# Optimization experiments

Measured on AMD Instinct MI355X. Metric: run time of the kernel, lower is better.

## Reference

```python
import jax, jax.numpy as jnp
import numpy as np

B, K, DIM = 8, 256, 50257
KNN, N_CLASS = 8, 4
KNN_T = 0.05


def setup_inputs() -> dict:
    key = jax.random.key(0)
    k1, k2, k3 = jax.random.split(key, 3)
    # probability-like positive values so log() is finite (KL-style distance)
    logits = jax.random.uniform(k1, (B, DIM), jnp.float32, minval=1e-3, maxval=1.0)
    queue_anchor = jax.random.uniform(k2, (B, K, DIM), jnp.float32, minval=1e-3, maxval=1.0)
    queue_label = jax.random.randint(k3, (B, K), 0, N_CLASS)  # int32 labels in [0, N_CLASS)
    return {"logits": logits, "queue_anchor": queue_anchor, "queue_label": queue_label}


def reference(logits, queue_anchor, queue_label):
    # KL-style distance over the vocab dim: dists[b,k] = mean_d qa[b,k,d]*(log qa[b,k,d] - log logits[b,d])
    log_logits = jnp.log(logits)  # [B, DIM]
    dists = jnp.mean(queue_anchor * (jnp.log(queue_anchor) - log_logits[:, None, :]), axis=2)  # [B, K]
    scaled_dists = (-1.0 / KNN_T) * dists
    top_dists, top_indices = jax.lax.top_k(scaled_dists, KNN)  # [B, KNN]
    top_values = jnp.take_along_axis(queue_label, top_indices, axis=1)  # [B, KNN] class ids
    knn_weight = jax.nn.softmax(top_dists, axis=-1)  # [B, KNN]
    # scatter weight into class bins then sum over neighbors == weighted one-hot sum
    knn_prob = jnp.sum(jax.nn.one_hot(top_values, N_CLASS, dtype=knn_weight.dtype) * knn_weight[..., None], axis=1)  # [B, N_CLASS]
    return knn_prob
```

## Files before the change

### kernel.cpp

```cpp
#include <hip/hip_runtime.h>
#include <math.h>

#define BATCH 8
#define KQ 256
#define DIM 50257
#define KNN 8
#define N_CLASS 4
#define INV_T 20.0f
#define LLSTRIDE 50264

__global__ __launch_bounds__(256) void log_logits_kernel(
        const float* __restrict__ logits, float* __restrict__ ll4, int n) {
    int i = blockIdx.x * 256 + threadIdx.x;
    if (i >= n) return;
    int b = i / DIM;
    int d = i - b * DIM;
    float v = __logf(logits[i]);
    #pragma unroll
    for (int c = 0; c < 4; ++c)
        ll4[((size_t)(c * BATCH + b)) * LLSTRIDE + c + d] = v;
}

__global__ __launch_bounds__(256) void dists_kernel(
        const float* __restrict__ qa, const float* __restrict__ ll4,
        float* __restrict__ dists) {
    const int bk = blockIdx.x;
    const int b  = bk >> 8;
    const int c  = bk & 3;
    const float* __restrict__ qrow = qa  + (size_t)bk * DIM;
    const float* __restrict__ lrow = ll4 + ((size_t)(c * BATCH + b)) * LLSTRIDE + c;

    const int peel = (4 - c) & 3;
    const int nv   = (DIM - peel) >> 2;
    const int tail = peel + nv * 4;
    const int t = threadIdx.x;

    float ax = 0.f, ay = 0.f, az = 0.f, aw = 0.f;
    const float4* __restrict__ q4 = (const float4*)(qrow + peel);
    const float4* __restrict__ l4 = (const float4*)(lrow + peel);
    for (int i = t; i < nv; i += 256) {
        float4 q = q4[i];
        float4 l = l4[i];
        ax += q.x * (__logf(q.x) - l.x);
        ay += q.y * (__logf(q.y) - l.y);
        az += q.z * (__logf(q.z) - l.z);
        aw += q.w * (__logf(q.w) - l.w);
    }
    float s = (ax + ay) + (az + aw);

    if (t < peel) {
        float q = qrow[t];
        s += q * (__logf(q) - lrow[t]);
    }
    int tn = DIM - tail;
    if (t >= 4 && t < 4 + tn) {
        int d = tail + (t - 4);
        float q = qrow[d];
        s += q * (__logf(q) - lrow[d]);
    }

    for (int o = 32; o > 0; o >>= 1) s += __shfl_xor(s, o, 64);
    __shared__ float part[4];
    if ((t & 63) == 0) part[t >> 6] = s;
    __syncthreads();
    if (t == 0) {
        float tot = (part[0] + part[1]) + (part[2] + part[3]);
        dists[bk] = tot * (1.0f / (float)DIM);
    }
}

__global__ __launch_bounds__(64) void topk_kernel(
        const float* __restrict__ dists, const int* __restrict__ labels,
        float* __restrict__ out) {
    const int b = blockIdx.x;
    const int lane = threadIdx.x;
    const int base = lane * 4;
    const float* __restrict__ drow = dists + b * KQ;

    float v[4];
    #pragma unroll
    for (int j = 0; j < 4; ++j) v[j] = -INV_T * drow[base + j];

    float topv[KNN]; int topi[KNN];
    #pragma unroll
    for (int it = 0; it < KNN; ++it) {
        float lv = v[0]; int li = base;
        #pragma unroll
        for (int j = 1; j < 4; ++j)
            if (v[j] > lv || (v[j] == lv && base + j < li)) { lv = v[j]; li = base + j; }
        #pragma unroll
        for (int o = 32; o > 0; o >>= 1) {
            float ov = __shfl_xor(lv, o, 64);
            int   oi = __shfl_xor(li, o, 64);
            if (ov > lv || (ov == lv && oi < li)) { lv = ov; li = oi; }
        }
        topv[it] = lv; topi[it] = li;
        if (li >= base && li < base + 4) v[li - base] = -INFINITY;
    }

    if (lane == 0) {
        float m = topv[0];
        float w[KNN], sum = 0.f;
        #pragma unroll
        for (int i = 0; i < KNN; ++i) { w[i] = __expf(topv[i] - m); sum += w[i]; }
        float p[N_CLASS] = {0.f, 0.f, 0.f, 0.f};
        #pragma unroll
        for (int i = 0; i < KNN; ++i) p[labels[b * KQ + topi[i]]] += w[i];
        float inv = 1.0f / sum;
        #pragma unroll
        for (int c = 0; c < N_CLASS; ++c) out[b * N_CLASS + c] = p[c] * inv;
    }
}

extern "C" void kernel_launch(void* const* d_in, const int* in_sizes, int n_in,
                              void* d_out, int out_size, void* d_ws, size_t ws_size,
                              hipStream_t stream) {
    const float* logits = (const float*)d_in[0];
    const float* qa     = (const float*)d_in[1];
    const int*   labels = (const int*)d_in[2];
    float* out = (float*)d_out;

    float* ll4   = (float*)d_ws;
    float* dists = ll4 + (size_t)4 * BATCH * LLSTRIDE;

    const int n_ll = BATCH * DIM;
    log_logits_kernel<<<(n_ll + 255) / 256, 256, 0, stream>>>(logits, ll4, n_ll);
    dists_kernel<<<BATCH * KQ, 256, 0, stream>>>(qa, ll4, dists);
    topk_kernel<<<BATCH, 64, 0, stream>>>(dists, labels, out);
}
```

Measured before the change: 557.5 us.

## Halve log-logits copies, use nontemporal loads, and unroll dists loop 4x

Measured after the change: 535.7 us. 1.04x faster.

```diff
diff --git a/kernel.cpp b/kernel.cpp
--- a/kernel.cpp
+++ b/kernel.cpp
@@ -7,28 +7,35 @@
 #define KNN 8
 #define N_CLASS 4
 #define INV_T 20.0f
-#define LLSTRIDE 50264
+#define LL2STRIDE 50260
+
+typedef float vf4 __attribute__((ext_vector_type(4)));
+
+__device__ __forceinline__ vf4 nt_load4(const float* p) {
+    return __builtin_nontemporal_load((const vf4*)p);
+}
 
 __global__ __launch_bounds__(256) void log_logits_kernel(
-        const float* __restrict__ logits, float* __restrict__ ll4, int n) {
+        const float* __restrict__ logits, float* __restrict__ ll2, int n) {
     int i = blockIdx.x * 256 + threadIdx.x;
     if (i >= n) return;
     int b = i / DIM;
     int d = i - b * DIM;
     float v = __logf(logits[i]);
     #pragma unroll
-    for (int c = 0; c < 4; ++c)
-        ll4[((size_t)(c * BATCH + b)) * LLSTRIDE + c + d] = v;
+    for (int s = 0; s < 2; ++s)
+        ll2[((size_t)(s * BATCH + b)) * LL2STRIDE + s + d] = v;
 }
 
 __global__ __launch_bounds__(256) void dists_kernel(
-        const float* __restrict__ qa, const float* __restrict__ ll4,
+        const float* __restrict__ qa, const float* __restrict__ ll2,
         float* __restrict__ dists) {
     const int bk = blockIdx.x;
     const int b  = bk >> 8;
     const int c  = bk & 3;
-    const float* __restrict__ qrow = qa  + (size_t)bk * DIM;
-    const float* __restrict__ lrow = ll4 + ((size_t)(c * BATCH + b)) * LLSTRIDE + c;
+    const int s  = bk & 1;
+    const float* __restrict__ qrow  = qa  + (size_t)bk * DIM;
+    const float* __restrict__ lrow2 = ll2 + ((size_t)(s * BATCH + b)) * LL2STRIDE + s;
 
     const int peel = (4 - c) & 3;
     const int nv   = (DIM - peel) >> 2;
@@ -36,32 +43,60 @@
     const int t = threadIdx.x;
 
     float ax = 0.f, ay = 0.f, az = 0.f, aw = 0.f;
-    const float4* __restrict__ q4 = (const float4*)(qrow + peel);
-    const float4* __restrict__ l4 = (const float4*)(lrow + peel);
-    for (int i = t; i < nv; i += 256) {
-        float4 q = q4[i];
-        float4 l = l4[i];
-        ax += q.x * (__logf(q.x) - l.x);
-        ay += q.y * (__logf(q.y) - l.y);
-        az += q.z * (__logf(q.z) - l.z);
-        aw += q.w * (__logf(q.w) - l.w);
+    const float*  __restrict__ qbase = qrow + peel;
+    const float2* __restrict__ l2 = (const float2*)(lrow2 + peel);
+
+    int i = t;
+    for (; i + 768 < nv; i += 1024) {
+        vf4 q0 = nt_load4(qbase + 4 * i);
+        vf4 q1 = nt_load4(qbase + 4 * (i + 256));
+        vf4 q2 = nt_load4(qbase + 4 * (i + 512));
+        vf4 q3 = nt_load4(qbase + 4 * (i + 768));
+        float2 l0a = l2[2 * i],             l0b = l2[2 * i + 1];
+        float2 l1a = l2[2 * (i + 256)],     l1b = l2[2 * (i + 256) + 1];
+        float2 l2a = l2[2 * (i + 512)],     l2b = l2[2 * (i + 512) + 1];
+        float2 l3a = l2[2 * (i + 768)],     l3b = l2[2 * (i + 768) + 1];
+        ax += q0.x * (__logf(q0.x) - l0a.x);
+        ay += q0.y * (__logf(q0.y) - l0a.y);
+        az += q0.z * (__logf(q0.z) - l0b.x);
+        aw += q0.w * (__logf(q0.w) - l0b.y);
+        ax += q1.x * (__logf(q1.x) - l1a.x);
+        ay += q1.y * (__logf(q1.y) - l1a.y);
+        az += q1.z * (__logf(q1.z) - l1b.x);
+        aw += q1.w * (__logf(q1.w) - l1b.y);
+        ax += q2.x * (__logf(q2.x) - l2a.x);
+        ay += q2.y * (__logf(q2.y) - l2a.y);
+        az += q2.z * (__logf(q2.z) - l2b.x);
+        aw += q2.w * (__logf(q2.w) - l2b.y);
+        ax += q3.x * (__logf(q3.x) - l3a.x);
+        ay += q3.y * (__logf(q3.y) - l3a.y);
+        az += q3.z * (__logf(q3.z) - l3b.x);
+        aw += q3.w * (__logf(q3.w) - l3b.y);
     }
-    float s = (ax + ay) + (az + aw);
+    for (; i < nv; i += 256) {
+        vf4 q = nt_load4(qbase + 4 * i);
+        float2 la = l2[2 * i], lb = l2[2 * i + 1];
+        ax += q.x * (__logf(q.x) - la.x);
+        ay += q.y * (__logf(q.y) - la.y);
+        az += q.z * (__logf(q.z) - lb.x);
+        aw += q.w * (__logf(q.w) - lb.y);
+    }
+    float sacc = (ax + ay) + (az + aw);
 
     if (t < peel) {
         float q = qrow[t];
-        s += q * (__logf(q) - lrow[t]);
+        sacc += q * (__logf(q) - lrow2[t]);
     }
     int tn = DIM - tail;
     if (t >= 4 && t < 4 + tn) {
         int d = tail + (t - 4);
         float q = qrow[d];
-        s += q * (__logf(q) - lrow[d]);
+        sacc += q * (__logf(q) - lrow2[d]);
     }
 
-    for (int o = 32; o > 0; o >>= 1) s += __shfl_xor(s, o, 64);
+    for (int o = 32; o > 0; o >>= 1) sacc += __shfl_xor(sacc, o, 64);
     __shared__ float part[4];
-    if ((t & 63) == 0) part[t >> 6] = s;
+    if ((t & 63) == 0) part[t >> 6] = sacc;
     __syncthreads();
     if (t == 0) {
         float tot = (part[0] + part[1]) + (part[2] + part[3]);
@@ -120,11 +155,11 @@
     const int*   labels = (const int*)d_in[2];
     float* out = (float*)d_out;
 
-    float* ll4   = (float*)d_ws;
-    float* dists = ll4 + (size_t)4 * BATCH * LLSTRIDE;
+    float* ll2   = (float*)d_ws;
+    float* dists = ll2 + (size_t)2 * BATCH * LL2STRIDE;
 
     const int n_ll = BATCH * DIM;
-    log_logits_kernel<<<(n_ll + 255) / 256, 256, 0, stream>>>(logits, ll4, n_ll);
-    dists_kernel<<<BATCH * KQ, 256, 0, stream>>>(qa, ll4, dists);
+    log_logits_kernel<<<(n_ll + 255) / 256, 256, 0, stream>>>(logits, ll2, n_ll);
+    dists_kernel<<<BATCH * KQ, 256, 0, stream>>>(qa, ll2, dists);
     topk_kernel<<<BATCH, 64, 0, stream>>>(dists, labels, out);
 }
```
